# Performance work log

Measured on AMD Instinct MI355X. Metric: run time of the kernel, lower is better.

## Reference

```python
import jax, jax.numpy as jnp
import numpy as np

N_GRAPHS = 16
NODES_PER = 420
N = N_GRAPHS * NODES_PER      # 6720 nodes
DEG = 8
E = N * DEG                   # 53760 edges
HEADS = 2
IN_DIM = 2048
H1 = 1024                     # conv1 out per head
H2 = 64                       # conv2 out (heads=1)
OUT_DIM = 18
SCALE = 0.02


def _lin(x, W, b):
    return x @ W + b


def _transformer_conv(x, src, dst, Wq, bq, Wk, bk, Wv, bv, Ws, bs, heads, d):
    # PyG TransformerConv: per-edge dot-product attention, softmax over incoming
    # edges of each destination node, scatter-sum of messages, + root skip.
    n = x.shape[0]
    q = _lin(x, Wq, bq).reshape(n, heads, d)
    k = _lin(x, Wk, bk).reshape(n, heads, d)
    v = _lin(x, Wv, bv).reshape(n, heads, d)
    alpha = (q[dst] * k[src]).sum(-1) / jnp.sqrt(jnp.asarray(d, x.dtype))  # [E, heads]
    amax = jax.ops.segment_max(alpha, dst, num_segments=n)
    ex = jnp.exp(alpha - amax[dst])
    denom = jax.ops.segment_sum(ex, dst, num_segments=n)
    a = ex / (denom[dst] + 1e-16)
    out = jax.ops.segment_sum(v[src] * a[..., None], dst, num_segments=n)  # [N, heads, d]
    return out.reshape(n, heads * d) + _lin(x, Ws, bs)


def setup_inputs() -> dict:
    key = jax.random.key(0)
    ks = jax.random.split(key, 32)
    x = jax.random.normal(ks[0], (N, IN_DIM), dtype=jnp.float32)
    dst = jax.random.randint(ks[1], (E,), 0, N)
    # keep edges within each 420-node graph
    src = (dst // NODES_PER) * NODES_PER + jax.random.randint(ks[2], (E,), 0, NODES_PER)
    edge_index = jnp.stack([src, dst]).astype(jnp.int64)  # [2, E]
    connectivity = jax.random.randint(ks[3], (N,), 1, 6).astype(jnp.int64)  # lobes 1..5
    p = lambda i, shape: SCALE * jax.random.normal(ks[i], shape, dtype=jnp.float32)
    inp = {
        'x': x, 'edge_index': edge_index, 'connectivity': connectivity,
        'node_pe': p(4, (NODES_PER, IN_DIM)),
        'lobe_pe': p(5, (5, IN_DIM)),
        'lung_pe': p(6, (2, IN_DIM)),
        'Wq1': p(7, (IN_DIM, HEADS * H1)), 'bq1': jnp.zeros((HEADS * H1,), jnp.float32),
        'Wk1': p(8, (IN_DIM, HEADS * H1)), 'bk1': jnp.zeros((HEADS * H1,), jnp.float32),
        'Wv1': p(9, (IN_DIM, HEADS * H1)), 'bv1': jnp.zeros((HEADS * H1,), jnp.float32),
        'Ws1': p(10, (IN_DIM, HEADS * H1)), 'bs1': jnp.zeros((HEADS * H1,), jnp.float32),
        'Wq2': p(11, (HEADS * H1, H2)), 'bq2': jnp.zeros((H2,), jnp.float32),
        'Wk2': p(12, (HEADS * H1, H2)), 'bk2': jnp.zeros((H2,), jnp.float32),
        'Wv2': p(13, (HEADS * H1, H2)), 'bv2': jnp.zeros((H2,), jnp.float32),
        'Ws2': p(14, (HEADS * H1, H2)), 'bs2': jnp.zeros((H2,), jnp.float32),
        'W_fc1': p(15, (NODES_PER * H2, 256)), 'b_fc1': jnp.zeros((256,), jnp.float32),
        'W_fc2': p(16, (256, 128)), 'b_fc2': jnp.zeros((128,), jnp.float32),
        'W_fc3': p(17, (128, 64)), 'b_fc3': jnp.zeros((64,), jnp.float32),
        'W_fc4': p(18, (64, OUT_DIM)), 'b_fc4': jnp.zeros((OUT_DIM,), jnp.float32),
    }
    return inp


def reference(x, edge_index, connectivity, node_pe, lobe_pe, lung_pe,
              Wq1, bq1, Wk1, bk1, Wv1, bv1, Ws1, bs1,
              Wq2, bq2, Wk2, bk2, Wv2, bv2, Ws2, bs2,
              W_fc1, b_fc1, W_fc2, b_fc2, W_fc3, b_fc3, W_fc4, b_fc4):
    src, dst = edge_index[0], edge_index[1]
    # positional embeddings: node PE tiled per graph, lobe PE (conn in 1..5),
    # lung PE (lobes 1,2 -> lung 0; lobes 3,4,5 -> lung 1)
    h = x + jnp.tile(node_pe, (N_GRAPHS, 1))
    h = h + lobe_pe[connectivity - 1]
    h = h + lung_pe[jnp.where(connectivity <= 2, 0, 1)]
    h = jax.nn.relu(_transformer_conv(h, src, dst, Wq1, bq1, Wk1, bk1, Wv1, bv1, Ws1, bs1, HEADS, H1))
    h = jax.nn.relu(_transformer_conv(h, src, dst, Wq2, bq2, Wk2, bk2, Wv2, bv2, Ws2, bs2, 1, H2))
    h = h.reshape(-1, NODES_PER * H2)  # [B, 420*64]
    h = jax.nn.relu(_lin(h, W_fc1, b_fc1))
    h = jax.nn.relu(_lin(h, W_fc2, b_fc2))
    h = jax.nn.relu(_lin(h, W_fc3, b_fc3))
    return _lin(h, W_fc4, b_fc4)
```

## Files before the change

kernel.cpp:

```cpp
#include <hip/hip_runtime.h>
#include <stdint.h>

#define N_GRAPHS 16
#define NODES_PER 420
#define NN (N_GRAPHS * NODES_PER)
#define MP 6784
#define EE (NN * 8)
#define IN_DIM 2048
#define NCAT1 8192
#define NCAT2 256
#define KDIM 2048

typedef __bf16 bf16x8 __attribute__((ext_vector_type(8)));
typedef float f32x4 __attribute__((ext_vector_type(4)));

__device__ __forceinline__ unsigned short f2bf(float f) {
  unsigned u = __float_as_uint(f);
  u += 0x7FFFu + ((u >> 16) & 1u);
  return (unsigned short)(u >> 16);
}
__device__ __forceinline__ float bf2f(unsigned short h) {
  return __uint_as_float(((unsigned)h) << 16);
}

__device__ __forceinline__ void gl2lds16(const void* g, const void* l) {
  __builtin_amdgcn_global_load_lds(
      (const __attribute__((address_space(1))) void*)(uintptr_t)g,
      (__attribute__((address_space(3))) void*)(unsigned int)(uintptr_t)l,
      16, 0, 0);
}

__global__ void prep_k(int* cnt, float* bcat1, float* bcat2, float* f1,
                       const float* bq1, const float* bk1, const float* bv1, const float* bs1,
                       const float* bq2, const float* bk2, const float* bv2, const float* bs2,
                       const float* bfc1) {
  int i = blockIdx.x * 256 + threadIdx.x;
  if (i < NN) cnt[i] = 0;
  if (i < NCAT1) {
    const float* p = i < 2048 ? bq1 : i < 4096 ? bk1 : i < 6144 ? bv1 : bs1;
    bcat1[i] = p[i & 2047];
  }
  if (i < NCAT2) {
    const float* p = i < 64 ? bq2 : i < 128 ? bk2 : i < 192 ? bv2 : bs2;
    bcat2[i] = p[i & 63];
  }
  if (i < 16 * 256) f1[i] = bfc1[i & 255];
}

__global__ void cnt_edges_k(const int* __restrict__ ei, int* __restrict__ cnt) {
  int e = blockIdx.x * 256 + threadIdx.x;
  if (e < EE) atomicAdd(&cnt[ei[EE + e]], 1);
}

__global__ void scan_offs_k(const int* __restrict__ cnt, int* __restrict__ offs,
                            int* __restrict__ cursor) {
  const int CH = 7;
  int t = threadIdx.x;
  int base = t * CH;
  int s = 0;
#pragma unroll
  for (int j = 0; j < CH; j++) { int idx = base + j; if (idx < NN) s += cnt[idx]; }
  __shared__ int sc[1024];
  sc[t] = s;
  __syncthreads();
  for (int d = 1; d < 1024; d <<= 1) {
    int v = 0;
    if (t >= d) v = sc[t - d];
    __syncthreads();
    if (t >= d) sc[t] += v;
    __syncthreads();
  }
  int run = sc[t] - s;
#pragma unroll
  for (int j = 0; j < CH; j++) {
    int idx = base + j;
    if (idx < NN) { offs[idx] = run; cursor[idx] = run; run += cnt[idx]; }
  }
  if (t == 1023) offs[NN] = run;
}

__global__ void scatter_k(const int* __restrict__ ei, int* __restrict__ cursor,
                          int* __restrict__ psrc) {
  int e = blockIdx.x * 256 + threadIdx.x;
  if (e < EE) {
    int d = ei[EE + e];
    int pos = atomicAdd(&cursor[d], 1);
    psrc[pos] = ei[e];
  }
}

__global__ void pe_add_k(const float* __restrict__ x, const int* __restrict__ conn,
                         const float* __restrict__ npe, const float* __restrict__ lpe,
                         const float* __restrict__ gpe, unsigned short* __restrict__ h0) {
  const int n = blockIdx.x, t = threadIdx.x;
  const int c = conn[n];
  const float4* x4 = (const float4*)(x + (size_t)n * IN_DIM);
  const float4* n4 = (const float4*)(npe + (size_t)(n % NODES_PER) * IN_DIM);
  const float4* l4 = (const float4*)(lpe + (size_t)(c - 1) * IN_DIM);
  const float4* g4 = (const float4*)(gpe + (size_t)(c <= 2 ? 0 : 1) * IN_DIM);
  ushort4* o4 = (ushort4*)(h0 + (size_t)n * IN_DIM);
#pragma unroll
  for (int i = 0; i < 2; i++) {
    int idx = i * 256 + t;
    float4 a = x4[idx], b = n4[idx], cc = l4[idx], d = g4[idx];
    ushort4 o;
    o.x = f2bf(a.x + b.x + cc.x + d.x);
    o.y = f2bf(a.y + b.y + cc.y + d.y);
    o.z = f2bf(a.z + b.z + cc.z + d.z);
    o.w = f2bf(a.w + b.w + cc.w + d.w);
    o4[idx] = o;
  }
}

__global__ void transw_k(const float* W0, const float* W1, const float* W2, const float* W3,
                         unsigned short* __restrict__ out, int K, int Ncol) {
  __shared__ float tile[32][33];
  const int z = blockIdx.z;
  const float* W = z == 0 ? W0 : z == 1 ? W1 : z == 2 ? W2 : W3;
  unsigned short* o = out + (size_t)z * Ncol * K;
  const int n0 = blockIdx.x * 32, k0 = blockIdx.y * 32;
  const int tx = threadIdx.x, ty = threadIdx.y;
#pragma unroll
  for (int r = 0; r < 4; r++)
    tile[ty + r * 8][tx] = W[(size_t)(k0 + ty + r * 8) * Ncol + n0 + tx];
  __syncthreads();
#pragma unroll
  for (int r = 0; r < 4; r++)
    o[(size_t)(n0 + ty + r * 8) * K + k0 + tx] = f2bf(tile[tx][ty + r * 8]);
}

template <int BM, int BN, int OUTF>
__launch_bounds__(256, 2)
__global__ void gemm_bt_k(const unsigned short* __restrict__ A,
                          const unsigned short* __restrict__ Bt,
                          const float* __restrict__ bias, void* __restrict__ C,
                          int Mlim, int Nsz, int K) {
  constexpr int BK = 32;
  constexpr int WTM = BM / 32, WTN = BN / 32;
  __shared__ __align__(16) unsigned short lA[BM * BK];
  __shared__ __align__(16) unsigned short lB[BN * BK];
  const int t = threadIdx.x;
  const int w = t >> 6, lane = t & 63;
  const int wm = w >> 1, wn = w & 1;
  const int quad = lane >> 4, l16 = lane & 15;
  const int m0 = blockIdx.y * BM, n0 = blockIdx.x * BN;

  f32x4 acc[WTM][WTN];
#pragma unroll
  for (int i = 0; i < WTM; i++)
#pragma unroll
    for (int j = 0; j < WTN; j++)
#pragma unroll
      for (int r = 0; r < 4; r++) acc[i][j][r] = 0.f;

  const int srow = t >> 2;
  const int scol = (t & 3) * 8;
  const unsigned short* Ab = A + (size_t)(m0 + srow) * K + scol;
  const unsigned short* Bb = Bt + (size_t)(n0 + srow) * K + scol;

  for (int k0 = 0; k0 < K; k0 += BK) {
    __syncthreads();
#pragma unroll
    for (int r = 0; r < BM / 64; r++)
      gl2lds16(Ab + (size_t)r * 64 * K + k0, (const char*)lA + r * 4096 + t * 16);
#pragma unroll
    for (int r = 0; r < BN / 64; r++)
      gl2lds16(Bb + (size_t)r * 64 * K + k0, (const char*)lB + r * 4096 + t * 16);
    __syncthreads();

    bf16x8 afr[WTM], bfr[WTN];
#pragma unroll
    for (int i = 0; i < WTM; i++) {
      int row = wm * (BM / 2) + i * 16 + l16;
      afr[i] = __builtin_bit_cast(bf16x8, *(const int4*)(&lA[row * 32 + quad * 8]));
    }
#pragma unroll
    for (int j = 0; j < WTN; j++) {
      int row = wn * (BN / 2) + j * 16 + l16;
      bfr[j] = __builtin_bit_cast(bf16x8, *(const int4*)(&lB[row * 32 + quad * 8]));
    }
#pragma unroll
    for (int i = 0; i < WTM; i++)
#pragma unroll
      for (int j = 0; j < WTN; j++)
        acc[i][j] = __builtin_amdgcn_mfma_f32_16x16x32_bf16(afr[i], bfr[j], acc[i][j], 0, 0, 0);
  }

#pragma unroll
  for (int j = 0; j < WTN; j++) {
    const int col = n0 + wn * (BN / 2) + j * 16 + l16;
    const float bs = bias[col];
#pragma unroll
    for (int i = 0; i < WTM; i++) {
#pragma unroll
      for (int r = 0; r < 4; r++) {
        int row = m0 + wm * (BM / 2) + i * 16 + quad * 4 + r;
        if (row < Mlim) {
          float v = acc[i][j][r] + bs;
          if constexpr (OUTF)
            ((float*)C)[(size_t)row * Nsz + col] = v;
          else
            ((unsigned short*)C)[(size_t)row * Nsz + col] = f2bf(v);
        }
      }
    }
  }
}

__global__ __launch_bounds__(256) void attn1_k(const unsigned short* __restrict__ qkvs,
                                               const int* __restrict__ offs,
                                               const int* __restrict__ psrc,
                                               unsigned short* __restrict__ h1) {
  const int n = blockIdx.x, t = threadIdx.x;
  const int w = t >> 6, lane = t & 63;
  __shared__ float s_q[2048];
  __shared__ float s_al[64][2];
  __shared__ int s_src[64];
  __shared__ float s_m[2], s_l[2], s_sc[2];
  const size_t rq = (size_t)n * NCAT1;
  float acc[8];
#pragma unroll
  for (int i = 0; i < 8; i++) {
    s_q[i * 256 + t] = bf2f(qkvs[rq + i * 256 + t]);
    acc[i] = 0.f;
  }
  if (t < 2) { s_m[t] = -1e30f; s_l[t] = 0.f; }
  __syncthreads();
  const int e0 = offs[n], e1 = offs[n + 1];
  for (int c0 = e0; c0 < e1; c0 += 64) {
    const int ce = min(64, e1 - c0);
    if (t < ce) s_src[t] = psrc[c0 + t];
    __syncthreads();
    for (int e = w; e < ce; e += 4) {
      const size_t kb = (size_t)s_src[e] * NCAT1 + 2048;
      float p0 = 0.f, p1 = 0.f;
#pragma unroll
      for (int i = 0; i < 16; i++) p0 += s_q[i * 64 + lane] * bf2f(qkvs[kb + i * 64 + lane]);
#pragma unroll
      for (int i = 16; i < 32; i++) p1 += s_q[i * 64 + lane] * bf2f(qkvs[kb + i * 64 + lane]);
#pragma unroll
      for (int s = 32; s > 0; s >>= 1) {
        p0 += __shfl_xor(p0, s, 64);
        p1 += __shfl_xor(p1, s, 64);
      }
      if (lane == 0) { s_al[e][0] = p0 * 0.03125f; s_al[e][1] = p1 * 0.03125f; }
    }
    __syncthreads();
    if (t < 2) {
      float mo = s_m[t], mn = mo;
      for (int e = 0; e < ce; e++) mn = fmaxf(mn, s_al[e][t]);
      float sc = __expf(mo - mn);
      float l = s_l[t] * sc;
      for (int e = 0; e < ce; e++) {
        float we = __expf(s_al[e][t] - mn);
        l += we;
        s_al[e][t] = we;
      }
      s_m[t] = mn; s_l[t] = l; s_sc[t] = sc;
    }
    __syncthreads();
#pragma unroll
    for (int i = 0; i < 8; i++) acc[i] *= s_sc[i >> 2];
    for (int e = 0; e < ce; e++) {
      const size_t vb = (size_t)s_src[e] * NCAT1 + 4096;
      const float w0 = s_al[e][0], w1 = s_al[e][1];
#pragma unroll
      for (int i = 0; i < 8; i++)
        acc[i] += (i < 4 ? w0 : w1) * bf2f(qkvs[vb + i * 256 + t]);
    }
    __syncthreads();
  }
#pragma unroll
  for (int i = 0; i < 8; i++) {
    float inv = 1.f / (s_l[i >> 2] + 1e-16f);
    float v = acc[i] * inv + bf2f(qkvs[rq + 6144 + i * 256 + t]);
    h1[(size_t)n * 2048 + i * 256 + t] = f2bf(fmaxf(v, 0.f));
  }
}

__global__ __launch_bounds__(64) void attn2_k(const float* __restrict__ qkvs2,
                                              const int* __restrict__ offs,
                                              const int* __restrict__ psrc,
                                              float* __restrict__ h2) {
  const int n = blockIdx.x, t = threadIdx.x;
  const size_t rb = (size_t)n * NCAT2;
  const float q = qkvs2[rb + t];
  float m = -1e30f, l = 0.f, acc = 0.f;
  const int e0 = offs[n], e1 = offs[n + 1];
  for (int e = e0; e < e1; e++) {
    const int src = psrc[e];
    float p = q * qkvs2[(size_t)src * NCAT2 + 64 + t];
#pragma unroll
    for (int s = 32; s > 0; s >>= 1) p += __shfl_xor(p, s, 64);
    p *= 0.125f;
    const float mn = fmaxf(m, p);
    const float sc = __expf(m - mn), we = __expf(p - mn);
    const float v = qkvs2[(size_t)src * NCAT2 + 128 + t];
    l = l * sc + we;
    acc = acc * sc + we * v;
    m = mn;
  }
  float o = acc / (l + 1e-16f) + qkvs2[rb + 192 + t];
  h2[(size_t)n * 64 + t] = fmaxf(o, 0.f);
}

__global__ __launch_bounds__(256) void fc1_k(const float* __restrict__ h2,
                                             const float* __restrict__ W,
                                             float* __restrict__ f1) {
  __shared__ float sA[16][256];
  const int t = threadIdx.x, k0 = blockIdx.x * 256;
#pragma unroll
  for (int r = 0; r < 16; r++) sA[r][t] = h2[(size_t)r * 26880 + k0 + t];
  __syncthreads();
  float acc[16];
#pragma unroll
  for (int r = 0; r < 16; r++) acc[r] = 0.f;
  for (int kk = 0; kk < 256; kk++) {
    const float wv = W[(size_t)(k0 + kk) * 256 + t];
#pragma unroll
    for (int r = 0; r < 16; r++) acc[r] += sA[r][kk] * wv;
  }
#pragma unroll
  for (int r = 0; r < 16; r++) atomicAdd(&f1[r * 256 + t], acc[r]);
}

__global__ void fc2_k(const float* __restrict__ f1, const float* __restrict__ W,
                      const float* __restrict__ b, float* __restrict__ f2) {
  const int t = threadIdx.x;
  const int j = t & 127, row = blockIdx.x * 2 + (t >> 7);
  float acc = 0.f;
  for (int k = 0; k < 256; k++) acc += fmaxf(f1[row * 256 + k], 0.f) * W[k * 128 + j];
  f2[row * 128 + j] = fmaxf(acc + b[j], 0.f);
}

__global__ void fc3_k(const float* __restrict__ f2, const float* __restrict__ W,
                      const float* __restrict__ b, float* __restrict__ f3) {
  const int t = threadIdx.x;
  const int j = t & 63, row = blockIdx.x * 4 + (t >> 6);
  float acc = 0.f;
  for (int k = 0; k < 128; k++) acc += f2[row * 128 + k] * W[k * 64 + j];
  f3[row * 64 + j] = fmaxf(acc + b[j], 0.f);
}

__global__ void fc4_k(const float* __restrict__ f3, const float* __restrict__ W,
                      const float* __restrict__ b, float* __restrict__ out) {
  const int t = threadIdx.x;
  if (t >= 16 * 18) return;
  const int row = t / 18, j = t % 18;
  float acc = 0.f;
  for (int k = 0; k < 64; k++) acc += f3[row * 64 + k] * W[k * 18 + j];
  out[t] = acc + b[j];
}

extern "C" void kernel_launch(void* const* d_in, const int* in_sizes, int n_in,
                              void* d_out, int out_size, void* d_ws, size_t ws_size,
                              hipStream_t stream) {
  const float* x    = (const float*)d_in[0];
  const int*   ei   = (const int*)d_in[1];
  const int*   conn = (const int*)d_in[2];
  const float* npe  = (const float*)d_in[3];
  const float* lpe  = (const float*)d_in[4];
  const float* gpe  = (const float*)d_in[5];
  const float* Wq1 = (const float*)d_in[6];  const float* bq1 = (const float*)d_in[7];
  const float* Wk1 = (const float*)d_in[8];  const float* bk1 = (const float*)d_in[9];
  const float* Wv1 = (const float*)d_in[10]; const float* bv1 = (const float*)d_in[11];
  const float* Ws1 = (const float*)d_in[12]; const float* bs1 = (const float*)d_in[13];
  const float* Wq2 = (const float*)d_in[14]; const float* bq2 = (const float*)d_in[15];
  const float* Wk2 = (const float*)d_in[16]; const float* bk2 = (const float*)d_in[17];
  const float* Wv2 = (const float*)d_in[18]; const float* bv2 = (const float*)d_in[19];
  const float* Ws2 = (const float*)d_in[20]; const float* bs2 = (const float*)d_in[21];
  const float* Wf1 = (const float*)d_in[22]; const float* bf1 = (const float*)d_in[23];
  const float* Wf2 = (const float*)d_in[24]; const float* bf2 = (const float*)d_in[25];
  const float* Wf3 = (const float*)d_in[26]; const float* bf3 = (const float*)d_in[27];
  const float* Wf4 = (const float*)d_in[28]; const float* bf4 = (const float*)d_in[29];
  float* out = (float*)d_out;

  char* ws = (char*)d_ws;
  size_t off = 0;
  auto alloc = [&](size_t bytes) -> void* {
    void* p = ws + off;
    off += (bytes + 255) & ~(size_t)255;
    return p;
  };
  unsigned short* h0    = (unsigned short*)alloc((size_t)MP * IN_DIM * 2);
  unsigned short* w1t   = (unsigned short*)alloc((size_t)NCAT1 * KDIM * 2);
  unsigned short* qkvs1 = (unsigned short*)alloc((size_t)MP * NCAT1 * 2);
  unsigned short* w2t   = (unsigned short*)alloc((size_t)NCAT2 * KDIM * 2);
  float* qkvs2 = (float*)alloc((size_t)MP * NCAT2 * 4);
  float* h2    = (float*)alloc((size_t)NN * 64 * 4);
  float* bcat1 = (float*)alloc(NCAT1 * 4);
  float* bcat2 = (float*)alloc(NCAT2 * 4);
  float* f1    = (float*)alloc(16 * 256 * 4);
  float* f2    = (float*)alloc(16 * 128 * 4);
  float* f3    = (float*)alloc(16 * 64 * 4);
  int* cnt    = (int*)alloc(NN * 4);
  int* offs   = (int*)alloc((NN + 1) * 4);
  int* cursor = (int*)alloc(NN * 4);
  int* psrc   = (int*)alloc(EE * 4);
  unsigned short* h1 = w1t;

  prep_k<<<32, 256, 0, stream>>>(cnt, bcat1, bcat2, f1,
                                 bq1, bk1, bv1, bs1, bq2, bk2, bv2, bs2, bf1);
  cnt_edges_k<<<EE / 256, 256, 0, stream>>>(ei, cnt);
  scan_offs_k<<<1, 1024, 0, stream>>>(cnt, offs, cursor);
  scatter_k<<<EE / 256, 256, 0, stream>>>(ei, cursor, psrc);
  pe_add_k<<<NN, 256, 0, stream>>>(x, conn, npe, lpe, gpe, h0);
  transw_k<<<dim3(64, 64, 4), dim3(32, 8), 0, stream>>>(Wq1, Wk1, Wv1, Ws1, w1t, KDIM, 2048);
  transw_k<<<dim3(2, 64, 4), dim3(32, 8), 0, stream>>>(Wq2, Wk2, Wv2, Ws2, w2t, KDIM, 64);
  gemm_bt_k<128, 128, 0><<<dim3(NCAT1 / 128, MP / 128), 256, 0, stream>>>(
      h0, w1t, bcat1, qkvs1, NN, NCAT1, KDIM);
  attn1_k<<<NN, 256, 0, stream>>>(qkvs1, offs, psrc, h1);
  gemm_bt_k<64, 64, 1><<<dim3(NCAT2 / 64, MP / 64), 256, 0, stream>>>(
      h1, w2t, bcat2, qkvs2, NN, NCAT2, KDIM);
  attn2_k<<<NN, 64, 0, stream>>>(qkvs2, offs, psrc, h2);
  fc1_k<<<26880 / 256, 256, 0, stream>>>(h2, Wf1, f1);
  fc2_k<<<8, 256, 0, stream>>>(f1, Wf2, bf2, f2);
  fc3_k<<<4, 256, 0, stream>>>(f2, Wf3, bf3, f3);
  fc4_k<<<1, 320, 0, stream>>>(f3, Wf4, bf4, out);
}
```

Before: 711.4 us.

## Swizzle GEMM LDS, group-tile block order, split attention per head, fuse FC tail

The GEMM now stages tiles in LDS with an XOR swizzle to avoid bank conflicts, walks blocks in 8-row stripes for better L2 reuse, raises the occupancy hint to 3, and drops the row bound check, so it now writes padded rows. The first attention kernel launches one block per node per head, loads q/k/v with vector reads, and maps blocks so each XCD handles whole graphs for cache locality. The second attention kernel gets the same XCD-aware node mapping. The fc2, fc3 and fc4 kernels are merged into one kernel, removing two launches and their intermediate buffers.

```diff
diff --git a/kernel.cpp b/kernel.cpp
--- a/kernel.cpp
+++ b/kernel.cpp
@@ -13,6 +13,7 @@
 
 typedef __bf16 bf16x8 __attribute__((ext_vector_type(8)));
 typedef float f32x4 __attribute__((ext_vector_type(4)));
+typedef unsigned short u16x8 __attribute__((ext_vector_type(8)));
 
 __device__ __forceinline__ unsigned short f2bf(float f) {
   unsigned u = __float_as_uint(f);
@@ -130,11 +131,11 @@
 }
 
 template <int BM, int BN, int OUTF>
-__launch_bounds__(256, 2)
+__launch_bounds__(256, 3)
 __global__ void gemm_bt_k(const unsigned short* __restrict__ A,
                           const unsigned short* __restrict__ Bt,
                           const float* __restrict__ bias, void* __restrict__ C,
-                          int Mlim, int Nsz, int K) {
+                          int Mblks, int Nsz, int K) {
   constexpr int BK = 32;
   constexpr int WTM = BM / 32, WTN = BN / 32;
   __shared__ __align__(16) unsigned short lA[BM * BK];
@@ -143,7 +144,15 @@
   const int w = t >> 6, lane = t & 63;
   const int wm = w >> 1, wn = w & 1;
   const int quad = lane >> 4, l16 = lane & 15;
-  const int m0 = blockIdx.y * BM, n0 = blockIdx.x * BN;
+
+  const int NB = Nsz / BN;
+  const int lin = blockIdx.x;
+  const int stripe = lin / (8 * NB);
+  const int rem = lin - stripe * 8 * NB;
+  const int hh = min(8, Mblks - stripe * 8);
+  const int mb = stripe * 8 + rem % hh;
+  const int nb = rem / hh;
+  const int m0 = mb * BM, n0 = nb * BN;
 
   f32x4 acc[WTM][WTN];
 #pragma unroll
@@ -154,7 +163,7 @@
       for (int r = 0; r < 4; r++) acc[i][j][r] = 0.f;
 
   const int srow = t >> 2;
-  const int scol = (t & 3) * 8;
+  const int scol = (((t & 3) ^ ((srow + (srow >> 2)) & 3)) * 8);
   const unsigned short* Ab = A + (size_t)(m0 + srow) * K + scol;
   const unsigned short* Bb = Bt + (size_t)(n0 + srow) * K + scol;
 
@@ -172,12 +181,14 @@
 #pragma unroll
     for (int i = 0; i < WTM; i++) {
       int row = wm * (BM / 2) + i * 16 + l16;
-      afr[i] = __builtin_bit_cast(bf16x8, *(const int4*)(&lA[row * 32 + quad * 8]));
+      int sw = quad ^ ((row + (row >> 2)) & 3);
+      afr[i] = __builtin_bit_cast(bf16x8, *(const int4*)(&lA[row * 32 + sw * 8]));
     }
 #pragma unroll
     for (int j = 0; j < WTN; j++) {
       int row = wn * (BN / 2) + j * 16 + l16;
-      bfr[j] = __builtin_bit_cast(bf16x8, *(const int4*)(&lB[row * 32 + quad * 8]));
+      int sw = quad ^ ((row + (row >> 2)) & 3);
+      bfr[j] = __builtin_bit_cast(bf16x8, *(const int4*)(&lB[row * 32 + sw * 8]));
     }
 #pragma unroll
     for (int i = 0; i < WTM; i++)
@@ -195,13 +206,11 @@
 #pragma unroll
       for (int r = 0; r < 4; r++) {
         int row = m0 + wm * (BM / 2) + i * 16 + quad * 4 + r;
-        if (row < Mlim) {
-          float v = acc[i][j][r] + bs;
-          if constexpr (OUTF)
-            ((float*)C)[(size_t)row * Nsz + col] = v;
-          else
-            ((unsigned short*)C)[(size_t)row * Nsz + col] = f2bf(v);
-        }
+        float v = acc[i][j][r] + bs;
+        if constexpr (OUTF)
+          ((float*)C)[(size_t)row * Nsz + col] = v;
+        else
+          ((unsigned short*)C)[(size_t)row * Nsz + col] = f2bf(v);
       }
     }
   }
@@ -211,20 +220,22 @@
                                                const int* __restrict__ offs,
                                                const int* __restrict__ psrc,
                                                unsigned short* __restrict__ h1) {
-  const int n = blockIdx.x, t = threadIdx.x;
-  const int w = t >> 6, lane = t & 63;
-  __shared__ float s_q[2048];
-  __shared__ float s_al[64][2];
+  const int bid = blockIdx.x;
+  const int xcd = bid & 7, idx = bid >> 3;
+  const int head = idx / 840;
+  const int r2 = idx - head * 840;
+  const int g = xcd * 2 + r2 / 420;
+  const int n = g * 420 + r2 % 420;
+  const int t = threadIdx.x, w = t >> 6, lane = t & 63;
+  __shared__ __align__(16) unsigned short s_q[1024];
+  __shared__ float s_al[64];
   __shared__ int s_src[64];
-  __shared__ float s_m[2], s_l[2], s_sc[2];
-  const size_t rq = (size_t)n * NCAT1;
-  float acc[8];
-#pragma unroll
-  for (int i = 0; i < 8; i++) {
-    s_q[i * 256 + t] = bf2f(qkvs[rq + i * 256 + t]);
-    acc[i] = 0.f;
-  }
-  if (t < 2) { s_m[t] = -1e30f; s_l[t] = 0.f; }
+  __shared__ float s_m, s_l, s_sc;
+  const size_t base = (size_t)n * NCAT1;
+  const size_t ho = (size_t)head * 1024;
+  *(ushort4*)(s_q + t * 4) = *(const ushort4*)(qkvs + base + ho + t * 4);
+  float acc[4] = {0.f, 0.f, 0.f, 0.f};
+  if (t == 0) { s_m = -1e30f; s_l = 0.f; }
   __syncthreads();
   const int e0 = offs[n], e1 = offs[n + 1];
   for (int c0 = e0; c0 < e1; c0 += 64) {
@@ -232,57 +243,66 @@
     if (t < ce) s_src[t] = psrc[c0 + t];
     __syncthreads();
     for (int e = w; e < ce; e += 4) {
-      const size_t kb = (size_t)s_src[e] * NCAT1 + 2048;
-      float p0 = 0.f, p1 = 0.f;
-#pragma unroll
-      for (int i = 0; i < 16; i++) p0 += s_q[i * 64 + lane] * bf2f(qkvs[kb + i * 64 + lane]);
-#pragma unroll
-      for (int i = 16; i < 32; i++) p1 += s_q[i * 64 + lane] * bf2f(qkvs[kb + i * 64 + lane]);
-#pragma unroll
-      for (int s = 32; s > 0; s >>= 1) {
-        p0 += __shfl_xor(p0, s, 64);
-        p1 += __shfl_xor(p1, s, 64);
+      const unsigned short* kp = qkvs + (size_t)s_src[e] * NCAT1 + 2048 + ho;
+      float p = 0.f;
+#pragma unroll
+      for (int i = 0; i < 2; i++) {
+        u16x8 kv = *(const u16x8*)(kp + i * 512 + lane * 8);
+        u16x8 qv = *(const u16x8*)(s_q + i * 512 + lane * 8);
+#pragma unroll
+        for (int j = 0; j < 8; j++) p += bf2f(qv[j]) * bf2f(kv[j]);
       }
-      if (lane == 0) { s_al[e][0] = p0 * 0.03125f; s_al[e][1] = p1 * 0.03125f; }
-    }
-    __syncthreads();
-    if (t < 2) {
-      float mo = s_m[t], mn = mo;
-      for (int e = 0; e < ce; e++) mn = fmaxf(mn, s_al[e][t]);
+#pragma unroll
+      for (int s = 32; s > 0; s >>= 1) p += __shfl_xor(p, s, 64);
+      if (lane == 0) s_al[e] = p * 0.03125f;
+    }
+    __syncthreads();
+    if (t == 0) {
+      float mo = s_m, mn = mo;
+      for (int e = 0; e < ce; e++) mn = fmaxf(mn, s_al[e]);
       float sc = __expf(mo - mn);
-      float l = s_l[t] * sc;
+      float l = s_l * sc;
       for (int e = 0; e < ce; e++) {
-        float we = __expf(s_al[e][t] - mn);
+        float we = __expf(s_al[e] - mn);
         l += we;
-        s_al[e][t] = we;
+        s_al[e] = we;
       }
-      s_m[t] = mn; s_l[t] = l; s_sc[t] = sc;
-    }
-    __syncthreads();
-#pragma unroll
-    for (int i = 0; i < 8; i++) acc[i] *= s_sc[i >> 2];
+      s_m = mn; s_l = l; s_sc = sc;
+    }
+    __syncthreads();
+    const float sc = s_sc;
+#pragma unroll
+    for (int j = 0; j < 4; j++) acc[j] *= sc;
     for (int e = 0; e < ce; e++) {
-      const size_t vb = (size_t)s_src[e] * NCAT1 + 4096;
-      const float w0 = s_al[e][0], w1 = s_al[e][1];
-#pragma unroll
-      for (int i = 0; i < 8; i++)
-        acc[i] += (i < 4 ? w0 : w1) * bf2f(qkvs[vb + i * 256 + t]);
-    }
-    __syncthreads();
-  }
-#pragma unroll
-  for (int i = 0; i < 8; i++) {
-    float inv = 1.f / (s_l[i >> 2] + 1e-16f);
-    float v = acc[i] * inv + bf2f(qkvs[rq + 6144 + i * 256 + t]);
-    h1[(size_t)n * 2048 + i * 256 + t] = f2bf(fmaxf(v, 0.f));
-  }
+      const unsigned short* vp = qkvs + (size_t)s_src[e] * NCAT1 + 4096 + ho;
+      const float we = s_al[e];
+      ushort4 vv = *(const ushort4*)(vp + t * 4);
+      acc[0] += we * bf2f(vv.x);
+      acc[1] += we * bf2f(vv.y);
+      acc[2] += we * bf2f(vv.z);
+      acc[3] += we * bf2f(vv.w);
+    }
+    __syncthreads();
+  }
+  const float inv = 1.f / (s_l + 1e-16f);
+  ushort4 sk = *(const ushort4*)(qkvs + base + 6144 + ho + t * 4);
+  ushort4 o;
+  o.x = f2bf(fmaxf(acc[0] * inv + bf2f(sk.x), 0.f));
+  o.y = f2bf(fmaxf(acc[1] * inv + bf2f(sk.y), 0.f));
+  o.z = f2bf(fmaxf(acc[2] * inv + bf2f(sk.z), 0.f));
+  o.w = f2bf(fmaxf(acc[3] * inv + bf2f(sk.w), 0.f));
+  *(ushort4*)(h1 + (size_t)n * 2048 + ho + t * 4) = o;
 }
 
 __global__ __launch_bounds__(64) void attn2_k(const float* __restrict__ qkvs2,
                                               const int* __restrict__ offs,
                                               const int* __restrict__ psrc,
                                               float* __restrict__ h2) {
-  const int n = blockIdx.x, t = threadIdx.x;
+  const int bid = blockIdx.x;
+  const int xcd = bid & 7, idx = bid >> 3;
+  const int g = xcd * 2 + idx / 420;
+  const int n = g * 420 + idx % 420;
+  const int t = threadIdx.x;
   const size_t rb = (size_t)n * NCAT2;
   const float q = qkvs2[rb + t];
   float m = -1e30f, l = 0.f, acc = 0.f;
@@ -324,32 +344,28 @@
   for (int r = 0; r < 16; r++) atomicAdd(&f1[r * 256 + t], acc[r]);
 }
 
-__global__ void fc2_k(const float* __restrict__ f1, const float* __restrict__ W,
-                      const float* __restrict__ b, float* __restrict__ f2) {
-  const int t = threadIdx.x;
-  const int j = t & 127, row = blockIdx.x * 2 + (t >> 7);
+__global__ __launch_bounds__(128) void fc234_k(const float* __restrict__ f1,
+                                               const float* __restrict__ W2, const float* __restrict__ b2,
+                                               const float* __restrict__ W3, const float* __restrict__ b3,
+                                               const float* __restrict__ W4, const float* __restrict__ b4,
+                                               float* __restrict__ out) {
+  const int row = blockIdx.x, t = threadIdx.x;
+  __shared__ float s2[128], s3[64];
   float acc = 0.f;
-  for (int k = 0; k < 256; k++) acc += fmaxf(f1[row * 256 + k], 0.f) * W[k * 128 + j];
-  f2[row * 128 + j] = fmaxf(acc + b[j], 0.f);
-}
-
-__global__ void fc3_k(const float* __restrict__ f2, const float* __restrict__ W,
-                      const float* __restrict__ b, float* __restrict__ f3) {
-  const int t = threadIdx.x;
-  const int j = t & 63, row = blockIdx.x * 4 + (t >> 6);
-  float acc = 0.f;
-  for (int k = 0; k < 128; k++) acc += f2[row * 128 + k] * W[k * 64 + j];
-  f3[row * 64 + j] = fmaxf(acc + b[j], 0.f);
-}
-
-__global__ void fc4_k(const float* __restrict__ f3, const float* __restrict__ W,
-                      const float* __restrict__ b, float* __restrict__ out) {
-  const int t = threadIdx.x;
-  if (t >= 16 * 18) return;
-  const int row = t / 18, j = t % 18;
-  float acc = 0.f;
-  for (int k = 0; k < 64; k++) acc += f3[row * 64 + k] * W[k * 18 + j];
-  out[t] = acc + b[j];
+  for (int k = 0; k < 256; k++) acc += fmaxf(f1[row * 256 + k], 0.f) * W2[k * 128 + t];
+  s2[t] = fmaxf(acc + b2[t], 0.f);
+  __syncthreads();
+  if (t < 64) {
+    float a3 = 0.f;
+    for (int k = 0; k < 128; k++) a3 += s2[k] * W3[k * 64 + t];
+    s3[t] = fmaxf(a3 + b3[t], 0.f);
+  }
+  __syncthreads();
+  if (t < 18) {
+    float a4 = 0.f;
+    for (int k = 0; k < 64; k++) a4 += s3[k] * W4[k * 18 + t];
+    out[row * 18 + t] = a4 + b4[t];
+  }
 }
 
 extern "C" void kernel_launch(void* const* d_in, const int* in_sizes, int n_in,
@@ -391,8 +407,6 @@
   float* bcat1 = (float*)alloc(NCAT1 * 4);
   float* bcat2 = (float*)alloc(NCAT2 * 4);
   float* f1    = (float*)alloc(16 * 256 * 4);
-  float* f2    = (float*)alloc(16 * 128 * 4);
-  float* f3    = (float*)alloc(16 * 64 * 4);
   int* cnt    = (int*)alloc(NN * 4);
   int* offs   = (int*)alloc((NN + 1) * 4);
   int* cursor = (int*)alloc(NN * 4);
@@ -407,14 +421,12 @@
   pe_add_k<<<NN, 256, 0, stream>>>(x, conn, npe, lpe, gpe, h0);
   transw_k<<<dim3(64, 64, 4), dim3(32, 8), 0, stream>>>(Wq1, Wk1, Wv1, Ws1, w1t, KDIM, 2048);
   transw_k<<<dim3(2, 64, 4), dim3(32, 8), 0, stream>>>(Wq2, Wk2, Wv2, Ws2, w2t, KDIM, 64);
-  gemm_bt_k<128, 128, 0><<<dim3(NCAT1 / 128, MP / 128), 256, 0, stream>>>(
-      h0, w1t, bcat1, qkvs1, NN, NCAT1, KDIM);
-  attn1_k<<<NN, 256, 0, stream>>>(qkvs1, offs, psrc, h1);
-  gemm_bt_k<64, 64, 1><<<dim3(NCAT2 / 64, MP / 64), 256, 0, stream>>>(
-      h1, w2t, bcat2, qkvs2, NN, NCAT2, KDIM);
+  gemm_bt_k<128, 128, 0><<<(MP / 128) * (NCAT1 / 128), 256, 0, stream>>>(
+      h0, w1t, bcat1, qkvs1, MP / 128, NCAT1, KDIM);
+  attn1_k<<<2 * NN, 256, 0, stream>>>(qkvs1, offs, psrc, h1);
+  gemm_bt_k<64, 64, 1><<<(MP / 64) * (NCAT2 / 64), 256, 0, stream>>>(
+      h1, w2t, bcat2, qkvs2, MP / 64, NCAT2, KDIM);
   attn2_k<<<NN, 64, 0, stream>>>(qkvs2, offs, psrc, h2);
   fc1_k<<<26880 / 256, 256, 0, stream>>>(h2, Wf1, f1);
-  fc2_k<<<8, 256, 0, stream>>>(f1, Wf2, bf2, f2);
-  fc3_k<<<4, 256, 0, stream>>>(f2, Wf3, bf3, f3);
-  fc4_k<<<1, 320, 0, stream>>>(f3, Wf4, bf4, out);
-}
+  fc234_k<<<16, 128, 0, stream>>>(f1, Wf2, bf2, Wf3, bf3, Wf4, bf4, out);
+}
```

Result: faster. 661.2 us (-7.1%).
